# Optimization experiments

Hardware: AMD Instinct MI355X
Metric: run time of the kernel (lower is better)

The kernel has to match this reference:

```python
import jax, jax.numpy as jnp
import numpy as np

NEG_INF = -1e9  # same masked_fill constant as the torch module
ALPHA = 0.1     # LeakyReLU negative slope


def setup_inputs() -> dict:
    key = jax.random.key(0)
    k1, k2, k3, k4, k5 = jax.random.split(key, 5)
    B, N, Din, Dout = 8, 2048, 512, 512
    features = jax.random.normal(k1, (B, N, Din), dtype=jnp.float32)
    graph = jax.random.randint(k2, (B, N, N), 0, 2, dtype=jnp.int64)
    # xavier_uniform with gain=1.414: limit = gain*sqrt(6/(fan_in+fan_out))
    lim_w = 1.414 * np.sqrt(6.0 / (Din + Dout))
    w = jax.random.uniform(k3, (Din, Dout), jnp.float32, -lim_w, lim_w)
    lim_a = 1.414 * np.sqrt(6.0 / (Dout + 1))
    a1 = jax.random.uniform(k4, (Dout, 1), jnp.float32, -lim_a, lim_a)
    a2 = jax.random.uniform(k5, (Dout, 1), jnp.float32, -lim_a, lim_a)
    return {"features": features, "graph": graph, "w": w, "a1": a1, "a2": a2}


def reference(features, graph, w, a1, a2):
    # hidden: [B, N, Dout]
    hidden = jnp.einsum("bni,io->bno", features, w)
    s1 = hidden @ a1  # [B, N, 1] -> broadcasts over columns
    s2 = hidden @ a2  # [B, N, 1] -> transposed broadcasts over rows
    # e[b,i,j] = leaky_relu(s1[b,i] + s2[b,j])
    e = jax.nn.leaky_relu(s1 + jnp.swapaxes(s2, 1, 2), negative_slope=ALPHA)
    e = jnp.where(graph == 0, NEG_INF, e)
    attn = jax.nn.softmax(e, axis=-1)  # [B, N, N]; dropout p=0 -> identity
    h_prime = jnp.einsum("bij,bjo->bio", attn, hidden)
    return jax.nn.elu(h_prime)  # concat=True
```

## Files before the change

### kernel.cpp

```cpp
#include <hip/hip_runtime.h>
#include <math.h>

#define B_ 8
#define N_ 2048
#define D_ 512
#define NROWS (B_ * N_)
#define NEG_ALPHA 0.1f

typedef __bf16 bf16;
typedef __bf16 bf16x4 __attribute__((ext_vector_type(4)));
typedef __bf16 bf16x8 __attribute__((ext_vector_type(8)));
typedef float f32x4 __attribute__((ext_vector_type(4)));
typedef float f32x16 __attribute__((ext_vector_type(16)));

#define HTB_BATCH ((D_ / 32) * (N_ / 16) * 512)

__global__ __launch_bounds__(256) void k_prep(const float* __restrict__ W,
                                              bf16* __restrict__ Wt) {
  __shared__ float tile[64][65];
  const int din0 = blockIdx.y * 64, dout0 = blockIdx.x * 64;
  const int tx = threadIdx.x & 63, tg = threadIdx.x >> 6;
#pragma unroll
  for (int rr = 0; rr < 16; ++rr) {
    int dr = tg * 16 + rr;
    tile[dr][tx] = W[(size_t)(din0 + dr) * D_ + dout0 + tx];
  }
  __syncthreads();
#pragma unroll
  for (int rr = 0; rr < 4; ++rr) {
    int dl = rr * 16 + (threadIdx.x >> 4);
    int nl = (threadIdx.x & 15) * 4;
    bf16x4 v = {(bf16)tile[nl][dl], (bf16)tile[nl + 1][dl],
                (bf16)tile[nl + 2][dl], (bf16)tile[nl + 3][dl]};
    *(bf16x4*)&Wt[(size_t)(dout0 + dl) * D_ + din0 + nl] = v;
  }
}

__global__ __launch_bounds__(256) void k_wa(const float* __restrict__ W,
                                            const float* __restrict__ a1,
                                            const float* __restrict__ a2,
                                            float* __restrict__ wa1,
                                            float* __restrict__ wa2) {
  const int wv = threadIdx.x >> 6, lane = threadIdx.x & 63;
  const int row = blockIdx.x * 4 + wv;
  const float* wr = W + (size_t)row * D_;
  float d1 = 0.f, d2 = 0.f;
#pragma unroll
  for (int p = 0; p < 8; ++p) {
    int c = lane + p * 64;
    float w = wr[c];
    d1 = fmaf(w, a1[c], d1);
    d2 = fmaf(w, a2[c], d2);
  }
#pragma unroll
  for (int off = 32; off > 0; off >>= 1) {
    d1 += __shfl_down(d1, off, 64);
    d2 += __shfl_down(d2, off, 64);
  }
  if (lane == 0) {
    wa1[row] = d1;
    wa2[row] = d2;
  }
}

__global__ __launch_bounds__(256) void k_scores_x(const float* __restrict__ X,
                                                  const float* __restrict__ wa1,
                                                  const float* __restrict__ wa2,
                                                  float* __restrict__ s1,
                                                  float* __restrict__ s2,
                                                  const int* __restrict__ G,
                                                  unsigned int* __restrict__ GB) {
  const int wv = threadIdx.x >> 6, lane = threadIdx.x & 63;
  const int r = blockIdx.x * 4 + wv;
  const float* x = X + (size_t)r * D_;
  float d1 = 0.f, d2 = 0.f;
#pragma unroll
  for (int p = 0; p < 2; ++p) {
    int c = lane * 4 + p * 256;
    float4 xv = *(const float4*)&x[c];
    float4 w1 = *(const float4*)&wa1[c];
    float4 w2 = *(const float4*)&wa2[c];
    d1 += xv.x * w1.x + xv.y * w1.y + xv.z * w1.z + xv.w * w1.w;
    d2 += xv.x * w2.x + xv.y * w2.y + xv.z * w2.z + xv.w * w2.w;
  }
  {
    const size_t g = (size_t)blockIdx.x * 256 + threadIdx.x;
    const int* src = G + g * 32;
    unsigned int bits = 0;
#pragma unroll
    for (int p = 0; p < 8; ++p) {
      int4 v = *(const int4*)&src[p * 4];
      bits |= (unsigned)(v.x != 0) << (p * 4);
      bits |= (unsigned)(v.y != 0) << (p * 4 + 1);
      bits |= (unsigned)(v.z != 0) << (p * 4 + 2);
      bits |= (unsigned)(v.w != 0) << (p * 4 + 3);
    }
    GB[g] = bits;
  }
#pragma unroll
  for (int off = 32; off > 0; off >>= 1) {
    d1 += __shfl_down(d1, off, 64);
    d2 += __shfl_down(d2, off, 64);
  }
  if (lane == 0) {
    s1[r] = d1;
    s2[r] = d2;
  }
}

#define LDH 40

__global__ __launch_bounds__(256, 2) void k_hiddenT(const float* __restrict__ X,
                                                    const bf16* __restrict__ Wt,
                                                    bf16* __restrict__ HtB) {
  __shared__ bf16 As[128][LDH];
  __shared__ bf16 Bs[128][LDH];
  const int t = threadIdx.x;
  const int m0 = blockIdx.y * 128;
  const int n0 = blockIdx.x * 128;
  const int lane = t & 63, w = t >> 6;
  const int wm = w >> 1, wn = w & 1;
  const int l15 = lane & 15, q = lane >> 4;

  f32x4 acc[4][4];
#pragma unroll
  for (int i = 0; i < 4; ++i)
#pragma unroll
    for (int j = 0; j < 4; ++j) acc[i][j] = (f32x4){0.f, 0.f, 0.f, 0.f};

  bf16x8 av[2];
  float4 bv[4];
#pragma unroll
  for (int p = 0; p < 2; ++p) {
    int s = t + p * 256;
    av[p] = *(const bf16x8*)&Wt[(size_t)(m0 + (s >> 2)) * D_ + (s & 3) * 8];
  }
#pragma unroll
  for (int p = 0; p < 4; ++p) {
    int s = t + p * 256;
    bv[p] = *(const float4*)&X[(size_t)(n0 + (s >> 3)) * D_ + (s & 7) * 4];
  }

  for (int k0 = 0; k0 < D_; k0 += 32) {
    __syncthreads();
#pragma unroll
    for (int p = 0; p < 2; ++p) {
      int s = t + p * 256;
      *(bf16x8*)&As[s >> 2][(s & 3) * 8] = av[p];
    }
#pragma unroll
    for (int p = 0; p < 4; ++p) {
      int s = t + p * 256;
      float4 v = bv[p];
      bf16x4 h = {(bf16)v.x, (bf16)v.y, (bf16)v.z, (bf16)v.w};
      *(bf16x4*)&Bs[s >> 3][(s & 7) * 4] = h;
    }
    __syncthreads();
    if (k0 + 32 < D_) {
#pragma unroll
      for (int p = 0; p < 2; ++p) {
        int s = t + p * 256;
        av[p] = *(const bf16x8*)&Wt[(size_t)(m0 + (s >> 2)) * D_ + k0 + 32 + (s & 3) * 8];
      }
#pragma unroll
      for (int p = 0; p < 4; ++p) {
        int s = t + p * 256;
        bv[p] = *(const float4*)&X[(size_t)(n0 + (s >> 3)) * D_ + k0 + 32 + (s & 7) * 4];
      }
    }
    bf16x8 a[4], bb[4];
#pragma unroll
    for (int i = 0; i < 4; ++i)
      a[i] = *(const bf16x8*)&As[wm * 64 + i * 16 + l15][q * 8];
#pragma unroll
    for (int j = 0; j < 4; ++j)
      bb[j] = *(const bf16x8*)&Bs[wn * 64 + j * 16 + l15][q * 8];
#pragma unroll
    for (int i = 0; i < 4; ++i)
#pragma unroll
      for (int j = 0; j < 4; ++j)
        acc[i][j] =
            __builtin_amdgcn_mfma_f32_16x16x32_bf16(a[i], bb[j], acc[i][j], 0, 0, 0);
  }
#pragma unroll
  for (int i = 0; i < 4; ++i)
#pragma unroll
    for (int r = 0; r < 4; ++r) {
      int dout = m0 + wm * 64 + i * 16 + q * 4 + r;
#pragma unroll
      for (int j = 0; j < 4; ++j) {
        int row = n0 + wn * 64 + j * 16 + l15;
        int bb_ = row >> 11;
        int jj = row & (N_ - 1);
        size_t addr = (size_t)bb_ * HTB_BATCH +
                      ((size_t)((dout >> 5) * (N_ / 16) + (jj >> 4)) * 64 +
                       ((jj >> 3) & 1) * 32 + (dout & 31)) *
                          8 +
                      (jj & 7);
        HtB[addr] = (bf16)acc[i][j][r];
      }
    }
}

#define AT_BM 64
#define AT_BK 32
#define LDP 40
#define NIT (N_ / AT_BK)
#define GROW 272

__global__ __launch_bounds__(512) void k_attn(const bf16* __restrict__ HtB,
                                              const unsigned char* __restrict__ GB,
                                              const float* __restrict__ s1,
                                              const float* __restrict__ s2,
                                              float* __restrict__ out) {
  __shared__ __align__(16) bf16 Ps[2][AT_BM][LDP];
  __shared__ __align__(16) bf16 Hs[2][16384];
  __shared__ float s2s[N_];
  __shared__ __align__(16) unsigned char gb_s[AT_BM][GROW];
  __shared__ float sum_part[AT_BM][8];
  __shared__ float row_sum[AT_BM];

  const int t = threadIdx.x;
  const int bid = blockIdx.x;
  const int b = bid & 7;
  const int i0 = (bid >> 3) * AT_BM;
  const int lane = t & 63, w = t >> 6;
  const int r31 = lane & 31, hf = lane >> 5;

  const bf16* Hb = HtB + (size_t)b * HTB_BATCH;
  const unsigned char* GBb = GB + ((size_t)b * N_ + i0) * (N_ / 8);

  for (int c = t; c < N_; c += 512) s2s[c] = s2[b * N_ + c];
  {
    int gr = t >> 3, gc = (t & 7) * 32;
    int4 w0 = *(const int4*)&GBb[(size_t)gr * (N_ / 8) + gc];
    int4 w1 = *(const int4*)&GBb[(size_t)gr * (N_ / 8) + gc + 16];
    *(int4*)&gb_s[gr][gc] = w0;
    *(int4*)&gb_s[gr][gc + 16] = w1;
  }

  const int pi = t >> 3;
  const int c8 = t & 7;
  const int pj = c8 * 4;
  const float s1r = s1[b * N_ + i0 + pi];
  float rsum = 0.f;

  f32x16 acc[2][2];
#pragma unroll
  for (int i = 0; i < 2; ++i)
#pragma unroll
    for (int j = 0; j < 2; ++j)
#pragma unroll
      for (int r = 0; r < 16; ++r) acc[i][j][r] = 0.f;

  bf16* HsF = &Hs[0][0];
#pragma unroll
  for (int nt = 0; nt < 2; ++nt)
#pragma unroll
    for (int jo = 0; jo < 2; ++jo) {
      const bf16* src =
          &Hb[((size_t)(w * 2 + nt) * (N_ / 16) + jo) * 512 + lane * 8];
      __builtin_amdgcn_global_load_lds(
          (const __attribute__((address_space(1))) void*)src,
          (__attribute__((address_space(3))) void*)
              &HsF[w * 2048 + (nt * 2 + jo) * 512],
          16, 0, 0);
    }

  __syncthreads();

#pragma unroll 1
  for (int it = 0; it < NIT; ++it) {
    const int cur = it & 1;
    {
      unsigned gbits = (unsigned)(gb_s[pi][it * 4 + (c8 >> 1)]) >> ((c8 & 1) * 4);
      f32x4 sv = *(const f32x4*)&s2s[it * AT_BK + pj];
      float pv[4];
#pragma unroll
      for (int q_ = 0; q_ < 4; ++q_) {
        float e = s1r + sv[q_];
        e = (e > 0.f) ? e : NEG_ALPHA * e;
        pv[q_] = ((gbits >> q_) & 1) ? __expf(e) : 0.f;
        rsum += pv[q_];
      }
      bf16x4 pb = {(bf16)pv[0], (bf16)pv[1], (bf16)pv[2], (bf16)pv[3]};
      *(bf16x4*)&Ps[cur][pi][pj] = pb;
    }
    {
      const int jn = (it + 1 < NIT) ? it + 1 : 0;
#pragma unroll
      for (int nt = 0; nt < 2; ++nt)
#pragma unroll
        for (int jo = 0; jo < 2; ++jo) {
          const bf16* src = &Hb[((size_t)(w * 2 + nt) * (N_ / 16) + jn * 2 + jo) *
                                    512 +
                                lane * 8];
          __builtin_amdgcn_global_load_lds(
              (const __attribute__((address_space(1))) void*)src,
              (__attribute__((address_space(3))) void*)
                  &HsF[(cur ^ 1) * 16384 + w * 2048 + (nt * 2 + jo) * 512],
              16, 0, 0);
        }
    }
    asm volatile("s_waitcnt lgkmcnt(0)" ::: "memory");
    __builtin_amdgcn_sched_barrier(0);
    __builtin_amdgcn_s_barrier();
    __builtin_amdgcn_sched_barrier(0);
    asm volatile("s_waitcnt vmcnt(4)" ::: "memory");
    __builtin_amdgcn_sched_barrier(0);
#pragma unroll
    for (int ks = 0; ks < 2; ++ks) {
      const int ko = ks * 16 + hf * 8;
      bf16x8 a0 = *(const bf16x8*)&Ps[cur][r31][ko];
      bf16x8 a1 = *(const bf16x8*)&Ps[cur][32 + r31][ko];
      bf16x8 b0 = *(const bf16x8*)&HsF[cur * 16384 + w * 2048 + ks * 512 + lane * 8];
      bf16x8 b1 =
          *(const bf16x8*)&HsF[cur * 16384 + w * 2048 + (2 + ks) * 512 + lane * 8];
      acc[0][0] = __builtin_amdgcn_mfma_f32_32x32x16_bf16(a0, b0, acc[0][0], 0, 0, 0);
      acc[0][1] = __builtin_amdgcn_mfma_f32_32x32x16_bf16(a0, b1, acc[0][1], 0, 0, 0);
      acc[1][0] = __builtin_amdgcn_mfma_f32_32x32x16_bf16(a1, b0, acc[1][0], 0, 0, 0);
      acc[1][1] = __builtin_amdgcn_mfma_f32_32x32x16_bf16(a1, b1, acc[1][1], 0, 0, 0);
    }
  }

  sum_part[pi][c8] = rsum;
  __syncthreads();
  if (t < AT_BM) {
    float s = 0.f;
#pragma unroll
    for (int k = 0; k < 8; ++k) s += sum_part[t][k];
    row_sum[t] = s;
  }
  __syncthreads();

#pragma unroll
  for (int mt = 0; mt < 2; ++mt) {
    float inv[16];
#pragma unroll
    for (int r = 0; r < 16; ++r)
      inv[r] = 1.f / row_sum[mt * 32 + (r & 3) + 8 * (r >> 2) + 4 * hf];
#pragma unroll
    for (int nt = 0; nt < 2; ++nt) {
      const int d = w * 64 + nt * 32 + r31;
#pragma unroll
      for (int r = 0; r < 16; ++r) {
        int i = mt * 32 + (r & 3) + 8 * (r >> 2) + 4 * hf;
        float x = acc[mt][nt][r] * inv[r];
        out[((size_t)b * N_ + i0 + i) * D_ + d] =
            (x > 0.f) ? x : (__expf(x) - 1.f);
      }
    }
  }
}

extern "C" void kernel_launch(void* const* d_in, const int* in_sizes, int n_in,
                              void* d_out, int out_size, void* d_ws,
                              size_t ws_size, hipStream_t stream) {
  const float* X = (const float*)d_in[0];
  const int* graph = (const int*)d_in[1];
  const float* W = (const float*)d_in[2];
  const float* a1 = (const float*)d_in[3];
  const float* a2 = (const float*)d_in[4];
  float* out = (float*)d_out;

  char* ws = (char*)d_ws;
  bf16* Wt = (bf16*)ws;
  bf16* HtB = (bf16*)(ws + (1 << 19));
  unsigned int* GBw = (unsigned int*)(ws + (1 << 19) + (16 << 20));
  float* s1 = (float*)(ws + (1 << 19) + (21 << 20));
  float* s2 = s1 + NROWS;
  float* wa1 = s2 + NROWS;
  float* wa2 = wa1 + D_;

  hipLaunchKernelGGL(k_prep, dim3(8, 8), dim3(256), 0, stream, W, Wt);
  hipLaunchKernelGGL(k_wa, dim3(128), dim3(256), 0, stream, W, a1, a2, wa1, wa2);
  hipLaunchKernelGGL(k_scores_x, dim3(NROWS / 4), dim3(256), 0, stream, X, wa1,
                     wa2, s1, s2, graph, GBw);
  hipLaunchKernelGGL(k_hiddenT, dim3(NROWS / 128, D_ / 128), dim3(256), 0,
                     stream, X, Wt, HtB);
  hipLaunchKernelGGL(k_attn, dim3(N_ / AT_BM * B_), dim3(512), 0, stream, HtB,
                     (const unsigned char*)GBw, s1, s2, out);
}
```

Baseline: 308.9 us.

## Fuse all stages into one cooperative kernel with grid-wide syncs

Replaces the five separate kernel launches (W transpose, W·a, score/bitmask pass, hidden GEMM, attention) with a single cooperative kernel of 256 blocks that uses grid syncs between phases. Each block builds its own graph bitmask rows directly in shared memory, computes s1/s2 and the bf16 hidden tile for its 64 rows, writes the tile to global, then runs the attention phase. This removes launch overhead and global round trips for the bitmask and s1. The cost is two grid-wide barriers, one block per CU, and a hidden GEMM split into small per-block tiles with less reuse. The graph read is no longer overlapped across a separate wide grid.

After: 511.5 us. +65.6%, slower.

```diff
diff --git a/kernel.cpp b/kernel.cpp
--- a/kernel.cpp
+++ b/kernel.cpp
@@ -1,5 +1,8 @@
 #include <hip/hip_runtime.h>
+#include <hip/hip_cooperative_groups.h>
 #include <math.h>
+
+namespace cg = cooperative_groups;
 
 #define B_ 8
 #define N_ 2048
@@ -15,234 +18,181 @@
 
 #define HTB_BATCH ((D_ / 32) * (N_ / 16) * 512)
 
-__global__ __launch_bounds__(256) void k_prep(const float* __restrict__ W,
-                                              bf16* __restrict__ Wt) {
-  __shared__ float tile[64][65];
-  const int din0 = blockIdx.y * 64, dout0 = blockIdx.x * 64;
-  const int tx = threadIdx.x & 63, tg = threadIdx.x >> 6;
-#pragma unroll
-  for (int rr = 0; rr < 16; ++rr) {
-    int dr = tg * 16 + rr;
-    tile[dr][tx] = W[(size_t)(din0 + dr) * D_ + dout0 + tx];
-  }
-  __syncthreads();
-#pragma unroll
-  for (int rr = 0; rr < 4; ++rr) {
-    int dl = rr * 16 + (threadIdx.x >> 4);
-    int nl = (threadIdx.x & 15) * 4;
-    bf16x4 v = {(bf16)tile[nl][dl], (bf16)tile[nl + 1][dl],
-                (bf16)tile[nl + 2][dl], (bf16)tile[nl + 3][dl]};
-    *(bf16x4*)&Wt[(size_t)(dout0 + dl) * D_ + din0 + nl] = v;
-  }
-}
-
-__global__ __launch_bounds__(256) void k_wa(const float* __restrict__ W,
-                                            const float* __restrict__ a1,
-                                            const float* __restrict__ a2,
-                                            float* __restrict__ wa1,
-                                            float* __restrict__ wa2) {
-  const int wv = threadIdx.x >> 6, lane = threadIdx.x & 63;
-  const int row = blockIdx.x * 4 + wv;
-  const float* wr = W + (size_t)row * D_;
-  float d1 = 0.f, d2 = 0.f;
-#pragma unroll
-  for (int p = 0; p < 8; ++p) {
-    int c = lane + p * 64;
-    float w = wr[c];
-    d1 = fmaf(w, a1[c], d1);
-    d2 = fmaf(w, a2[c], d2);
-  }
-#pragma unroll
-  for (int off = 32; off > 0; off >>= 1) {
-    d1 += __shfl_down(d1, off, 64);
-    d2 += __shfl_down(d2, off, 64);
-  }
-  if (lane == 0) {
-    wa1[row] = d1;
-    wa2[row] = d2;
-  }
-}
-
-__global__ __launch_bounds__(256) void k_scores_x(const float* __restrict__ X,
-                                                  const float* __restrict__ wa1,
-                                                  const float* __restrict__ wa2,
-                                                  float* __restrict__ s1,
-                                                  float* __restrict__ s2,
-                                                  const int* __restrict__ G,
-                                                  unsigned int* __restrict__ GB) {
-  const int wv = threadIdx.x >> 6, lane = threadIdx.x & 63;
-  const int r = blockIdx.x * 4 + wv;
-  const float* x = X + (size_t)r * D_;
-  float d1 = 0.f, d2 = 0.f;
-#pragma unroll
-  for (int p = 0; p < 2; ++p) {
-    int c = lane * 4 + p * 256;
-    float4 xv = *(const float4*)&x[c];
-    float4 w1 = *(const float4*)&wa1[c];
-    float4 w2 = *(const float4*)&wa2[c];
-    d1 += xv.x * w1.x + xv.y * w1.y + xv.z * w1.z + xv.w * w1.w;
-    d2 += xv.x * w2.x + xv.y * w2.y + xv.z * w2.z + xv.w * w2.w;
-  }
-  {
-    const size_t g = (size_t)blockIdx.x * 256 + threadIdx.x;
-    const int* src = G + g * 32;
-    unsigned int bits = 0;
-#pragma unroll
-    for (int p = 0; p < 8; ++p) {
-      int4 v = *(const int4*)&src[p * 4];
-      bits |= (unsigned)(v.x != 0) << (p * 4);
-      bits |= (unsigned)(v.y != 0) << (p * 4 + 1);
-      bits |= (unsigned)(v.z != 0) << (p * 4 + 2);
-      bits |= (unsigned)(v.w != 0) << (p * 4 + 3);
-    }
-    GB[g] = bits;
-  }
-#pragma unroll
-  for (int off = 32; off > 0; off >>= 1) {
-    d1 += __shfl_down(d1, off, 64);
-    d2 += __shfl_down(d2, off, 64);
-  }
-  if (lane == 0) {
-    s1[r] = d1;
-    s2[r] = d2;
-  }
-}
-
-#define LDH 40
-
-__global__ __launch_bounds__(256, 2) void k_hiddenT(const float* __restrict__ X,
-                                                    const bf16* __restrict__ Wt,
-                                                    bf16* __restrict__ HtB) {
-  __shared__ bf16 As[128][LDH];
-  __shared__ bf16 Bs[128][LDH];
-  const int t = threadIdx.x;
-  const int m0 = blockIdx.y * 128;
-  const int n0 = blockIdx.x * 128;
-  const int lane = t & 63, w = t >> 6;
-  const int wm = w >> 1, wn = w & 1;
-  const int l15 = lane & 15, q = lane >> 4;
-
-  f32x4 acc[4][4];
-#pragma unroll
-  for (int i = 0; i < 4; ++i)
-#pragma unroll
-    for (int j = 0; j < 4; ++j) acc[i][j] = (f32x4){0.f, 0.f, 0.f, 0.f};
-
-  bf16x8 av[2];
-  float4 bv[4];
-#pragma unroll
-  for (int p = 0; p < 2; ++p) {
-    int s = t + p * 256;
-    av[p] = *(const bf16x8*)&Wt[(size_t)(m0 + (s >> 2)) * D_ + (s & 3) * 8];
-  }
-#pragma unroll
-  for (int p = 0; p < 4; ++p) {
-    int s = t + p * 256;
-    bv[p] = *(const float4*)&X[(size_t)(n0 + (s >> 3)) * D_ + (s & 7) * 4];
-  }
-
-  for (int k0 = 0; k0 < D_; k0 += 32) {
-    __syncthreads();
-#pragma unroll
-    for (int p = 0; p < 2; ++p) {
-      int s = t + p * 256;
-      *(bf16x8*)&As[s >> 2][(s & 3) * 8] = av[p];
-    }
-#pragma unroll
-    for (int p = 0; p < 4; ++p) {
-      int s = t + p * 256;
-      float4 v = bv[p];
-      bf16x4 h = {(bf16)v.x, (bf16)v.y, (bf16)v.z, (bf16)v.w};
-      *(bf16x4*)&Bs[s >> 3][(s & 7) * 4] = h;
-    }
-    __syncthreads();
-    if (k0 + 32 < D_) {
-#pragma unroll
-      for (int p = 0; p < 2; ++p) {
-        int s = t + p * 256;
-        av[p] = *(const bf16x8*)&Wt[(size_t)(m0 + (s >> 2)) * D_ + k0 + 32 + (s & 3) * 8];
-      }
-#pragma unroll
-      for (int p = 0; p < 4; ++p) {
-        int s = t + p * 256;
-        bv[p] = *(const float4*)&X[(size_t)(n0 + (s >> 3)) * D_ + k0 + 32 + (s & 7) * 4];
-      }
-    }
-    bf16x8 a[4], bb[4];
-#pragma unroll
-    for (int i = 0; i < 4; ++i)
-      a[i] = *(const bf16x8*)&As[wm * 64 + i * 16 + l15][q * 8];
-#pragma unroll
-    for (int j = 0; j < 4; ++j)
-      bb[j] = *(const bf16x8*)&Bs[wn * 64 + j * 16 + l15][q * 8];
-#pragma unroll
-    for (int i = 0; i < 4; ++i)
-#pragma unroll
-      for (int j = 0; j < 4; ++j)
-        acc[i][j] =
-            __builtin_amdgcn_mfma_f32_16x16x32_bf16(a[i], bb[j], acc[i][j], 0, 0, 0);
-  }
-#pragma unroll
-  for (int i = 0; i < 4; ++i)
-#pragma unroll
-    for (int r = 0; r < 4; ++r) {
-      int dout = m0 + wm * 64 + i * 16 + q * 4 + r;
-#pragma unroll
-      for (int j = 0; j < 4; ++j) {
-        int row = n0 + wn * 64 + j * 16 + l15;
-        int bb_ = row >> 11;
-        int jj = row & (N_ - 1);
-        size_t addr = (size_t)bb_ * HTB_BATCH +
-                      ((size_t)((dout >> 5) * (N_ / 16) + (jj >> 4)) * 64 +
-                       ((jj >> 3) & 1) * 32 + (dout & 31)) *
-                          8 +
-                      (jj & 7);
-        HtB[addr] = (bf16)acc[i][j][r];
-      }
-    }
-}
-
-#define AT_BM 64
+#define WTB_CHUNKS ((D_ / 32) * (D_ / 16))
+
+#define XS_PITCH 520
 #define AT_BK 32
+#define NIT (N_ / AT_BK)
 #define LDP 40
-#define NIT (N_ / AT_BK)
 #define GROW 272
 
-__global__ __launch_bounds__(512) void k_attn(const bf16* __restrict__ HtB,
-                                              const unsigned char* __restrict__ GB,
-                                              const float* __restrict__ s1,
-                                              const float* __restrict__ s2,
-                                              float* __restrict__ out) {
-  __shared__ __align__(16) bf16 Ps[2][AT_BM][LDP];
-  __shared__ __align__(16) bf16 Hs[2][16384];
+__global__ __launch_bounds__(512, 1) void k_fused(
+    const float* __restrict__ X, const int* __restrict__ G,
+    const float* __restrict__ W, const float* __restrict__ a1,
+    const float* __restrict__ a2, float* __restrict__ wa1g,
+    float* __restrict__ wa2g, bf16* __restrict__ WtB, bf16* __restrict__ HtB,
+    float* __restrict__ s2g, float* __restrict__ out) {
+  __shared__ __align__(16) char u_mem[64 * XS_PITCH * 2];
+  __shared__ __align__(16) unsigned char gb_s[64][GROW];
   __shared__ float s2s[N_];
-  __shared__ __align__(16) unsigned char gb_s[AT_BM][GROW];
-  __shared__ float sum_part[AT_BM][8];
-  __shared__ float row_sum[AT_BM];
+  __shared__ __align__(16) bf16 Ps[2][64][LDP];
+  __shared__ float s1s[64];
+  __shared__ float sum_part[64][8];
+  __shared__ float row_sum[64];
 
   const int t = threadIdx.x;
   const int bid = blockIdx.x;
   const int b = bid & 7;
-  const int i0 = (bid >> 3) * AT_BM;
+  const int i0 = (bid >> 3) * 64;
   const int lane = t & 63, w = t >> 6;
   const int r31 = lane & 31, hf = lane >> 5;
 
+  if (w < 2) {
+    const int row = bid * 2 + w;
+    const float* wr = W + (size_t)row * D_;
+    float d1 = 0.f, d2 = 0.f;
+#pragma unroll
+    for (int p = 0; p < 8; ++p) {
+      int c = lane + p * 64;
+      float wv = wr[c];
+      d1 = fmaf(wv, a1[c], d1);
+      d2 = fmaf(wv, a2[c], d2);
+    }
+#pragma unroll
+    for (int off = 32; off > 0; off >>= 1) {
+      d1 += __shfl_down(d1, off, 64);
+      d2 += __shfl_down(d2, off, 64);
+    }
+    if (lane == 0) {
+      wa1g[row] = d1;
+      wa2g[row] = d2;
+    }
+  }
+  if (t < 128) {
+    const int c = bid * 2 + (t >> 6);
+    const int l = t & 63;
+    const int db = c >> 5, kc = c & 31;
+    const int dout = db * 32 + (l & 31);
+    const int dbase = kc * 16 + (l >> 5) * 8;
+    bf16 v[8];
+#pragma unroll
+    for (int e = 0; e < 8; ++e) v[e] = (bf16)W[(size_t)(dbase + e) * D_ + dout];
+    *(bf16x8*)&WtB[((size_t)c * 64 + l) * 8] = *(bf16x8*)v;
+  }
+  {
+    const int gr = t >> 3;
+    const int* grow = G + (size_t)(b * N_ + i0 + gr) * N_;
+    unsigned int* gw = (unsigned int*)&gb_s[gr][0];
+#pragma unroll 2
+    for (int s = 0; s < 8; ++s) {
+      const int widx = (t & 7) + s * 8;
+      const int* src = grow + widx * 32;
+      unsigned int bits = 0;
+#pragma unroll
+      for (int p = 0; p < 8; ++p) {
+        int4 v = *(const int4*)&src[p * 4];
+        bits |= (unsigned)(v.x != 0) << (p * 4);
+        bits |= (unsigned)(v.y != 0) << (p * 4 + 1);
+        bits |= (unsigned)(v.z != 0) << (p * 4 + 2);
+        bits |= (unsigned)(v.w != 0) << (p * 4 + 3);
+      }
+      gw[widx] = bits;
+    }
+  }
+  __threadfence();
+  cg::this_grid().sync();
+
+  bf16* Xs = (bf16*)u_mem;
+  {
+    float wl1[8], wl2[8];
+#pragma unroll
+    for (int e = 0; e < 8; ++e) {
+      wl1[e] = wa1g[lane * 8 + e];
+      wl2[e] = wa2g[lane * 8 + e];
+    }
+#pragma unroll
+    for (int q = 0; q < 8; ++q) {
+      const int rr = w * 8 + q;
+      const float* xr = X + (size_t)(b * N_ + i0 + rr) * D_;
+      float4 xa = *(const float4*)&xr[lane * 8];
+      float4 xb = *(const float4*)&xr[lane * 8 + 4];
+      float xv[8] = {xa.x, xa.y, xa.z, xa.w, xb.x, xb.y, xb.z, xb.w};
+      float d1 = 0.f, d2 = 0.f;
+      bf16 hv[8];
+#pragma unroll
+      for (int e = 0; e < 8; ++e) {
+        d1 = fmaf(xv[e], wl1[e], d1);
+        d2 = fmaf(xv[e], wl2[e], d2);
+        hv[e] = (bf16)xv[e];
+      }
+      *(bf16x8*)&Xs[rr * XS_PITCH + lane * 8] = *(bf16x8*)hv;
+#pragma unroll
+      for (int off = 32; off > 0; off >>= 1) {
+        d1 += __shfl_down(d1, off, 64);
+        d2 += __shfl_down(d2, off, 64);
+      }
+      if (lane == 0) {
+        s1s[rr] = d1;
+        s2g[b * N_ + i0 + rr] = d2;
+      }
+    }
+  }
+  __syncthreads();
+
+  {
+    f32x16 hacc[2][2];
+#pragma unroll
+    for (int i = 0; i < 2; ++i)
+#pragma unroll
+      for (int j = 0; j < 2; ++j)
+#pragma unroll
+        for (int r = 0; r < 16; ++r) hacc[i][j][r] = 0.f;
+
+#pragma unroll 4
+    for (int kc = 0; kc < 32; ++kc) {
+      bf16x8 aF[2], bF[2];
+#pragma unroll
+      for (int rt = 0; rt < 2; ++rt)
+        aF[rt] = *(const bf16x8*)&Xs[(rt * 32 + r31) * XS_PITCH + kc * 16 + hf * 8];
+#pragma unroll
+      for (int nt = 0; nt < 2; ++nt)
+        bF[nt] = *(const bf16x8*)&WtB[(((size_t)(w * 2 + nt) * 32 + kc) * 64 + lane) * 8];
+#pragma unroll
+      for (int rt = 0; rt < 2; ++rt)
+#pragma unroll
+        for (int nt = 0; nt < 2; ++nt)
+          hacc[rt][nt] = __builtin_amdgcn_mfma_f32_32x32x16_bf16(
+              aF[rt], bF[nt], hacc[rt][nt], 0, 0, 0);
+    }
+    bf16* Hb = HtB + (size_t)b * HTB_BATCH;
+#pragma unroll
+    for (int rt = 0; rt < 2; ++rt)
+#pragma unroll
+      for (int nt = 0; nt < 2; ++nt) {
+        const int dout = (w * 2 + nt) * 32 + r31;
+#pragma unroll
+        for (int r = 0; r < 16; ++r) {
+          const int J = i0 + rt * 32 + (r & 3) + 8 * (r >> 2) + 4 * hf;
+          size_t addr = ((size_t)((dout >> 5) * (N_ / 16) + (J >> 4)) * 64 +
+                         ((J >> 3) & 1) * 32 + (dout & 31)) *
+                            8 +
+                        (J & 7);
+          Hb[addr] = (bf16)hacc[rt][nt][r];
+        }
+      }
+  }
+  __threadfence();
+  cg::this_grid().sync();
+
+  bf16* HsF = (bf16*)u_mem;
   const bf16* Hb = HtB + (size_t)b * HTB_BATCH;
-  const unsigned char* GBb = GB + ((size_t)b * N_ + i0) * (N_ / 8);
-
-  for (int c = t; c < N_; c += 512) s2s[c] = s2[b * N_ + c];
-  {
-    int gr = t >> 3, gc = (t & 7) * 32;
-    int4 w0 = *(const int4*)&GBb[(size_t)gr * (N_ / 8) + gc];
-    int4 w1 = *(const int4*)&GBb[(size_t)gr * (N_ / 8) + gc + 16];
-    *(int4*)&gb_s[gr][gc] = w0;
-    *(int4*)&gb_s[gr][gc + 16] = w1;
-  }
+
+  for (int c = t; c < N_; c += 512) s2s[c] = s2g[b * N_ + c];
 
   const int pi = t >> 3;
   const int c8 = t & 7;
   const int pj = c8 * 4;
-  const float s1r = s1[b * N_ + i0 + pi];
+  const float s1r = s1s[pi];
   float rsum = 0.f;
 
   f32x16 acc[2][2];
@@ -253,7 +203,6 @@
 #pragma unroll
       for (int r = 0; r < 16; ++r) acc[i][j][r] = 0.f;
 
-  bf16* HsF = &Hs[0][0];
 #pragma unroll
   for (int nt = 0; nt < 2; ++nt)
 #pragma unroll
@@ -262,18 +211,18 @@
           &Hb[((size_t)(w * 2 + nt) * (N_ / 16) + jo) * 512 + lane * 8];
       __builtin_amdgcn_global_load_lds(
           (const __attribute__((address_space(1))) void*)src,
-          (__attribute__((address_space(3))) void*)
-              &HsF[w * 2048 + (nt * 2 + jo) * 512],
+          (__attribute__((address_space(3))) void*)&HsF[w * 2048 +
+                                                        (nt * 2 + jo) * 512],
           16, 0, 0);
     }
-
   __syncthreads();
 
 #pragma unroll 1
   for (int it = 0; it < NIT; ++it) {
     const int cur = it & 1;
     {
-      unsigned gbits = (unsigned)(gb_s[pi][it * 4 + (c8 >> 1)]) >> ((c8 & 1) * 4);
+      unsigned gbits =
+          (unsigned)(gb_s[pi][it * 4 + (c8 >> 1)]) >> ((c8 & 1) * 4);
       f32x4 sv = *(const f32x4*)&s2s[it * AT_BK + pj];
       float pv[4];
 #pragma unroll
@@ -297,8 +246,9 @@
                                 lane * 8];
           __builtin_amdgcn_global_load_lds(
               (const __attribute__((address_space(1))) void*)src,
-              (__attribute__((address_space(3))) void*)
-                  &HsF[(cur ^ 1) * 16384 + w * 2048 + (nt * 2 + jo) * 512],
+              (__attribute__((address_space(3))) void*)&HsF[(cur ^ 1) * 16384 +
+                                                            w * 2048 +
+                                                            (nt * 2 + jo) * 512],
               16, 0, 0);
         }
     }
@@ -325,7 +275,7 @@
 
   sum_part[pi][c8] = rsum;
   __syncthreads();
-  if (t < AT_BM) {
+  if (t < 64) {
     float s = 0.f;
 #pragma unroll
     for (int k = 0; k < 8; ++k) s += sum_part[t][k];
@@ -357,27 +307,20 @@
                               void* d_out, int out_size, void* d_ws,
                               size_t ws_size, hipStream_t stream) {
   const float* X = (const float*)d_in[0];
-  const int* graph = (const int*)d_in[1];
+  const int* G = (const int*)d_in[1];
   const float* W = (const float*)d_in[2];
   const float* a1 = (const float*)d_in[3];
   const float* a2 = (const float*)d_in[4];
   float* out = (float*)d_out;
 
   char* ws = (char*)d_ws;
-  bf16* Wt = (bf16*)ws;
-  bf16* HtB = (bf16*)(ws + (1 << 19));
-  unsigned int* GBw = (unsigned int*)(ws + (1 << 19) + (16 << 20));
-  float* s1 = (float*)(ws + (1 << 19) + (21 << 20));
-  float* s2 = s1 + NROWS;
-  float* wa1 = s2 + NROWS;
-  float* wa2 = wa1 + D_;
-
-  hipLaunchKernelGGL(k_prep, dim3(8, 8), dim3(256), 0, stream, W, Wt);
-  hipLaunchKernelGGL(k_wa, dim3(128), dim3(256), 0, stream, W, a1, a2, wa1, wa2);
-  hipLaunchKernelGGL(k_scores_x, dim3(NROWS / 4), dim3(256), 0, stream, X, wa1,
-                     wa2, s1, s2, graph, GBw);
-  hipLaunchKernelGGL(k_hiddenT, dim3(NROWS / 128, D_ / 128), dim3(256), 0,
-                     stream, X, Wt, HtB);
-  hipLaunchKernelGGL(k_attn, dim3(N_ / AT_BM * B_), dim3(512), 0, stream, HtB,
-                     (const unsigned char*)GBw, s1, s2, out);
+  bf16* WtB = (bf16*)ws;
+  bf16* HtB = (bf16*)(ws + (1 << 20));
+  float* wa1g = (float*)(ws + (1 << 20) + (16 << 20));
+  float* wa2g = wa1g + D_;
+  float* s2g = wa2g + D_;
+
+  void* args[] = {&X, &G, &W, &a1, &a2, &wa1g, &wa2g, &WtB, &HtB, &s2g, &out};
+  hipLaunchCooperativeKernel((const void*)k_fused, dim3(256), dim3(512), args,
+                             0, stream);
 }
```
